# Optimization experiments

Hardware: AMD Instinct MI355X
Metric: run time of the kernel (lower is better)

The kernel has to match this reference:

```python
import jax, jax.numpy as jnp
import numpy as np

EPS = 1e-5      # BatchNorm eps (torch default)
TEMP = 2.0      # initial_temperature
TOP_K = 2


def _bn(x, g, b, m, v):
    # eval-mode BatchNorm over channel dim of [B, C]
    return (x - m) * jax.lax.rsqrt(v + EPS) * g + b


def setup_inputs() -> dict:
    key = jax.random.key(0)
    ks = jax.random.split(key, 16)
    B, C, H, W, E = 64, 768, 32, 32, 16
    C2 = 2 * C            # 1536
    R = C2 // 16          # 96 (ChannelAttention bottleneck)
    s = 0.02
    f32 = jnp.float32
    return {
        "x": jax.random.normal(ks[0], (B, C, H, W), f32),
        # conv1x1 C->2C
        "w1": jax.random.normal(ks[1], (C2, C), f32) * s,
        "b1": jnp.zeros((C2,), f32),
        # BN(2C)
        "bn1_g": jnp.ones((C2,), f32),
        "bn1_b": jnp.zeros((C2,), f32),
        "bn1_m": jax.random.normal(ks[2], (C2,), f32) * 0.1,
        "bn1_v": jax.random.uniform(ks[3], (C2,), f32, 0.5, 1.5),
        # ChannelAttention fc: 2C -> 2C/16 -> 2C
        "caw1": jax.random.normal(ks[4], (R, C2), f32) * s,
        "cab1": jnp.zeros((R,), f32),
        "caw2": jax.random.normal(ks[5], (C2, R), f32) * s,
        "cab2": jnp.zeros((C2,), f32),
        # conv1x1 2C->C
        "w2": jax.random.normal(ks[6], (C, C2), f32) * s,
        "b2": jnp.zeros((C,), f32),
        # BN(C)
        "bn2_g": jnp.ones((C,), f32),
        "bn2_b": jnp.zeros((C,), f32),
        "bn2_m": jax.random.normal(ks[7], (C,), f32) * 0.1,
        "bn2_v": jax.random.uniform(ks[8], (C,), f32, 0.5, 1.5),
        # conv1x1 C->E
        "w3": jax.random.normal(ks[9], (E, C), f32) * s,
        "b3": jnp.zeros((E,), f32),
    }


def reference(x, w1, b1, bn1_g, bn1_b, bn1_m, bn1_v,
              caw1, cab1, caw2, cab2,
              w2, b2, bn2_g, bn2_b, bn2_m, bn2_v,
              w3, b3):
    # global avg pool: [B,C,H,W] -> [B,C] (1x1 spatial squeezed)
    g = jnp.mean(x, axis=(2, 3))
    # conv1x1 C->2C + BN + GELU (exact erf gelu, torch default)
    h = jax.nn.gelu(_bn(g @ w1.T + b1, bn1_g, bn1_b, bn1_m, bn1_v),
                    approximate=False)
    # ChannelAttention on 1x1 feature map: avg_pool == max_pool == identity,
    # so avg_out + max_out = 2 * fc(h)
    a = jax.nn.gelu(h @ caw1.T + cab1, approximate=False) @ caw2.T + cab2
    h = h * jax.nn.sigmoid(a + a)
    # conv1x1 2C->C + BN + GELU
    h = jax.nn.gelu(_bn(h @ w2.T + b2, bn2_g, bn2_b, bn2_m, bn2_v),
                    approximate=False)
    # conv1x1 C->E -> gating scores [B, E]
    scores = h @ w3.T + b3
    vals, idx = jax.lax.top_k(scores, TOP_K)
    probs = jax.nn.softmax(vals / TEMP, axis=1)
    return idx, probs
```

## Files before the change

kernel.cpp:

```cpp
#include <hip/hip_runtime.h>
#include <hip/hip_bf16.h>
#include <math.h>

#define B_   64
#define C_   768
#define C2_  1536
#define R_   96
#define E_   16
#define HW_  1024

typedef float f32x4 __attribute__((ext_vector_type(4)));

__device__ __forceinline__ float gelu_exact(float x) {
    return 0.5f * x * (1.0f + erff(x * 0.70710678118654752440f));
}

__device__ __forceinline__ f32x4 nt_load4(const float* p) {
    return __builtin_nontemporal_load(reinterpret_cast<const f32x4*>(p));
}

__global__ __launch_bounds__(256) void pool_kernel(const float* __restrict__ x,
                                                   float* __restrict__ gT) {
    const int wave = threadIdx.x >> 6;
    const int lane = threadIdx.x & 63;
    const int row  = blockIdx.x * 4 + wave;
    const int b = row / C_;
    const int c = row % C_;
    const float* p = x + (size_t)row * HW_;
    f32x4 a0 = nt_load4(p + lane * 4 +    0);
    f32x4 a1 = nt_load4(p + lane * 4 +  256);
    f32x4 a2 = nt_load4(p + lane * 4 +  512);
    f32x4 a3 = nt_load4(p + lane * 4 +  768);
    float s = (a0.x + a0.y + a0.z + a0.w) + (a1.x + a1.y + a1.z + a1.w)
            + (a2.x + a2.y + a2.z + a2.w) + (a3.x + a3.y + a3.z + a3.w);
    #pragma unroll
    for (int off = 32; off >= 1; off >>= 1) s += __shfl_xor(s, off);
    if (lane == 0) gT[c * B_ + b] = s * (1.0f / (float)HW_);
}

template<int K, bool BN>
__global__ __launch_bounds__(512) void gemv4_kernel(
    const float* __restrict__ inT,
    const float* __restrict__ W,
    const float* __restrict__ bias,
    const float* __restrict__ bn_g, const float* __restrict__ bn_b,
    const float* __restrict__ bn_m, const float* __restrict__ bn_v,
    float* __restrict__ outT)
{
    __shared__ __align__(16) float wl[4 * K];
    __shared__ float part[4][8][64];
    const int t  = threadIdx.x;
    const int c0 = blockIdx.x * 4;
    {
        const float* src = W + (size_t)c0 * K;
        f32x4* dst = reinterpret_cast<f32x4*>(wl);
        #pragma unroll
        for (int i = t; i < K; i += 512) dst[i] = nt_load4(src + i * 4);
    }
    __syncthreads();
    const int b = t & 63, w = t >> 6;
    const int kc = w * (K / 8);
    const float* w0 = wl + kc;
    const float* g  = inT + (size_t)kc * B_ + b;
    float a0 = 0.f, a1 = 0.f, a2 = 0.f, a3 = 0.f;
    #pragma unroll 8
    for (int k = 0; k < K / 8; ++k) {
        float gv = g[k * B_];
        a0 = fmaf(gv, w0[k],         a0);
        a1 = fmaf(gv, w0[K + k],     a1);
        a2 = fmaf(gv, w0[2 * K + k], a2);
        a3 = fmaf(gv, w0[3 * K + k], a3);
    }
    part[0][w][b] = a0;
    part[1][w][b] = a1;
    part[2][w][b] = a2;
    part[3][w][b] = a3;
    __syncthreads();
    if (t < 256) {
        const int ci = t >> 6, bb = t & 63, c = c0 + ci;
        float s = (part[ci][0][bb] + part[ci][1][bb])
                + (part[ci][2][bb] + part[ci][3][bb])
                + (part[ci][4][bb] + part[ci][5][bb])
                + (part[ci][6][bb] + part[ci][7][bb]);
        s += bias[c];
        if (BN) s = (s - bn_m[c]) * rsqrtf(bn_v[c] + 1e-5f) * bn_g[c] + bn_b[c];
        outT[(size_t)c * B_ + bb] = gelu_exact(s);
    }
}

__global__ __launch_bounds__(512) void l2_kernel(
    const float* __restrict__ h1T, const float* __restrict__ caw1,
    const float* __restrict__ cab1, float* __restrict__ rT)
{
    __shared__ __align__(16) float wl[C2_];
    __shared__ float part[8][64];
    const int t = threadIdx.x;
    const int c = blockIdx.x;
    {
        const float* src = caw1 + (size_t)c * C2_;
        f32x4* dst = reinterpret_cast<f32x4*>(wl);
        if (t < 384) dst[t] = nt_load4(src + t * 4);
    }
    __syncthreads();
    const int b = t & 63, w = t >> 6;
    const int kc = w * 192;
    const float* hp = h1T + (size_t)kc * B_ + b;
    float a0 = 0.f, a1 = 0.f, a2 = 0.f;
    #pragma unroll 8
    for (int k = 0; k < 64; ++k) {
        a0 = fmaf(hp[k * B_],         wl[kc + k],       a0);
        a1 = fmaf(hp[(k + 64) * B_],  wl[kc + k + 64],  a1);
        a2 = fmaf(hp[(k + 128) * B_], wl[kc + k + 128], a2);
    }
    part[w][b] = (a0 + a1) + a2;
    __syncthreads();
    if (t < 64) {
        float s = 0.f;
        #pragma unroll
        for (int ww = 0; ww < 8; ++ww) s += part[ww][t];
        rT[(size_t)c * B_ + t] = gelu_exact(s + cab1[c]);
    }
}

__global__ __launch_bounds__(512) void gate_kernel(
    const float* __restrict__ rT, const float* __restrict__ caw2,
    const float* __restrict__ cab2,
    const float* __restrict__ h1T, float* __restrict__ h1gT)
{
    const int t = threadIdx.x;
    const int b = t & 63, w = t >> 6;
    const int c = __builtin_amdgcn_readfirstlane(blockIdx.x * 8 + w);
    const float* wr = caw2 + (size_t)c * R_;
    const float* rp = rT + b;
    float a0 = 0.f, a1 = 0.f;
    #pragma unroll 8
    for (int k = 0; k < 48; ++k) {
        a0 = fmaf(rp[k * B_],        wr[k],      a0);
        a1 = fmaf(rp[(k + 48) * B_], wr[k + 48], a1);
    }
    float a = a0 + a1 + cab2[c];
    float sig = 1.0f / (1.0f + expf(-2.0f * a));
    h1gT[(size_t)c * B_ + b] = h1T[(size_t)c * B_ + b] * sig;
}

__global__ __launch_bounds__(256) void l5_kernel(
    const float* __restrict__ h2T, const float* __restrict__ w3,
    const float* __restrict__ b3, float* __restrict__ out)
{
    __shared__ float part[256];
    __shared__ float sc[E_];
    const int t = threadIdx.x;
    const int b = blockIdx.x;
    const int e = t & 15, kg = t >> 4;
    const float* wr = w3 + (size_t)e * C_ + kg * 48;
    const float* hv = h2T + (size_t)kg * 48 * B_ + b;
    float acc = 0.f;
    #pragma unroll 8
    for (int j = 0; j < 48; ++j) acc = fmaf(hv[j * B_], wr[j], acc);
    part[t] = acc;
    __syncthreads();
    if (t < E_) {
        float s = b3[t];
        #pragma unroll
        for (int kgi = 0; kgi < 16; ++kgi) s += part[kgi * 16 + t];
        sc[t] = s;
    }
    __syncthreads();
    if (t == 0) {
        int i0 = 0; float v0 = sc[0];
        #pragma unroll
        for (int i = 1; i < E_; ++i) { if (sc[i] > v0) { v0 = sc[i]; i0 = i; } }
        int i1 = -1; float v1 = -INFINITY;
        #pragma unroll
        for (int i = 0; i < E_; ++i) {
            if (i == i0) continue;
            if (sc[i] > v1) { v1 = sc[i]; i1 = i; }
        }
        float e1 = expf((v1 - v0) * 0.5f);
        float inv = 1.0f / (1.0f + e1);
        out[b * 2 + 0] = (float)i0;
        out[b * 2 + 1] = (float)i1;
        out[2 * B_ + b * 2 + 0] = inv;
        out[2 * B_ + b * 2 + 1] = e1 * inv;
    }
}

extern "C" void kernel_launch(void* const* d_in, const int* in_sizes, int n_in,
                              void* d_out, int out_size, void* d_ws, size_t ws_size,
                              hipStream_t stream) {
    const float* x     = (const float*)d_in[0];
    const float* w1    = (const float*)d_in[1];
    const float* b1    = (const float*)d_in[2];
    const float* bn1_g = (const float*)d_in[3];
    const float* bn1_b = (const float*)d_in[4];
    const float* bn1_m = (const float*)d_in[5];
    const float* bn1_v = (const float*)d_in[6];
    const float* caw1  = (const float*)d_in[7];
    const float* cab1  = (const float*)d_in[8];
    const float* caw2  = (const float*)d_in[9];
    const float* cab2  = (const float*)d_in[10];
    const float* w2    = (const float*)d_in[11];
    const float* b2    = (const float*)d_in[12];
    const float* bn2_g = (const float*)d_in[13];
    const float* bn2_b = (const float*)d_in[14];
    const float* bn2_m = (const float*)d_in[15];
    const float* bn2_v = (const float*)d_in[16];
    const float* w3    = (const float*)d_in[17];
    const float* b3    = (const float*)d_in[18];

    float* ws   = (float*)d_ws;
    float* gT   = ws;
    float* h1T  = ws + 49152;
    float* rT   = ws + 147456;
    float* h2T  = ws + 153600;
    float* h1gT = ws + 202752;
    float* out = (float*)d_out;

    pool_kernel<<<(B_ * C_) / 4, 256, 0, stream>>>(x, gT);
    gemv4_kernel<C_, true><<<C2_ / 4, 512, 0, stream>>>(
        gT, w1, b1, bn1_g, bn1_b, bn1_m, bn1_v, h1T);
    l2_kernel<<<R_, 512, 0, stream>>>(h1T, caw1, cab1, rT);
    gate_kernel<<<C2_ / 8, 512, 0, stream>>>(rT, caw2, cab2, h1T, h1gT);
    gemv4_kernel<C2_, true><<<C_ / 4, 512, 0, stream>>>(
        h1gT, w2, b2, bn2_g, bn2_b, bn2_m, bn2_v, h2T);
    l5_kernel<<<B_, 256, 0, stream>>>(h2T, w3, b3, out);
}
```

Measured before the change: 66.33 us.

## Fuse channel-attention layers into one per-batch kernel with pre-transposed caw2

Replaces the separate l2 and gate kernels with a single ca_gate_kernel that runs one block per batch row. The block stages h1 in shared memory, computes the 96-wide bottleneck with wave reductions, then applies the gate. The caw2 transpose it needs is folded into extra blocks of the pool kernel so it costs no extra launch. This removes one launch and the rT round trip. The trade-off is only 64 blocks, with each block rereading caw1 and caw2T, which lowers parallelism and raises L2 traffic. The old path is kept as a fallback when the workspace is too small.

```diff
diff --git a/kernel.cpp b/kernel.cpp
--- a/kernel.cpp
+++ b/kernel.cpp
@@ -8,6 +8,8 @@
 #define R_   96
 #define E_   16
 #define HW_  1024
+#define POOLB_ (B_ * C_ / 4)
+#define TRB_   24
 
 typedef float f32x4 __attribute__((ext_vector_type(4)));
 
@@ -20,7 +22,19 @@
 }
 
 __global__ __launch_bounds__(256) void pool_kernel(const float* __restrict__ x,
-                                                   float* __restrict__ gT) {
+                                                   float* __restrict__ gT,
+                                                   const float* __restrict__ caw2,
+                                                   float* __restrict__ caw2T) {
+    if (blockIdx.x >= POOLB_) {
+        const int base = (blockIdx.x - POOLB_) * 6144 + threadIdx.x;
+        #pragma unroll 4
+        for (int n = 0; n < 24; ++n) {
+            int idx = base + n * 256;
+            int k = idx / C2_, c = idx - k * C2_;
+            caw2T[idx] = caw2[(size_t)c * R_ + k];
+        }
+        return;
+    }
     const int wave = threadIdx.x >> 6;
     const int lane = threadIdx.x & 63;
     const int row  = blockIdx.x * 4 + wave;
@@ -40,8 +54,7 @@
 
 template<int K, bool BN>
 __global__ __launch_bounds__(512) void gemv4_kernel(
-    const float* __restrict__ inT,
-    const float* __restrict__ W,
+    const float* __restrict__ inT, const float* __restrict__ W,
     const float* __restrict__ bias,
     const float* __restrict__ bn_g, const float* __restrict__ bn_b,
     const float* __restrict__ bn_m, const float* __restrict__ bn_v,
@@ -88,6 +101,45 @@
     }
 }
 
+__global__ __launch_bounds__(512) void ca_gate_kernel(
+    const float* __restrict__ h1T,
+    const float* __restrict__ caw1, const float* __restrict__ cab1,
+    const float* __restrict__ caw2T, const float* __restrict__ cab2,
+    float* __restrict__ h1gT)
+{
+    __shared__ float h1l[C2_];
+    __shared__ float rl[R_];
+    const int t = threadIdx.x;
+    const int b = blockIdx.x;
+    #pragma unroll
+    for (int i = 0; i < 3; ++i) h1l[t + i * 512] = h1T[(size_t)(t + i * 512) * B_ + b];
+    __syncthreads();
+    const int w = t >> 6, l = t & 63;
+    #pragma unroll
+    for (int jj = 0; jj < 12; ++jj) {
+        const int j = w * 12 + jj;
+        const float* wr = caw1 + (size_t)j * C2_;
+        float acc = 0.f;
+        #pragma unroll 8
+        for (int m = 0; m < 24; ++m)
+            acc = fmaf(wr[l + 64 * m], h1l[l + 64 * m], acc);
+        #pragma unroll
+        for (int off = 32; off >= 1; off >>= 1) acc += __shfl_xor(acc, off);
+        if (l == 0) rl[j] = gelu_exact(acc + cab1[j]);
+    }
+    __syncthreads();
+    #pragma unroll
+    for (int cc = 0; cc < 3; ++cc) {
+        const int c = t + cc * 512;
+        float a = cab2[c];
+        #pragma unroll 8
+        for (int k = 0; k < R_; ++k)
+            a = fmaf(caw2T[(size_t)k * C2_ + c], rl[k], a);
+        float sig = 1.0f / (1.0f + expf(-2.0f * a));
+        h1gT[(size_t)c * B_ + b] = h1l[c] * sig;
+    }
+}
+
 __global__ __launch_bounds__(512) void l2_kernel(
     const float* __restrict__ h1T, const float* __restrict__ caw1,
     const float* __restrict__ cab1, float* __restrict__ rT)
@@ -96,11 +148,7 @@
     __shared__ float part[8][64];
     const int t = threadIdx.x;
     const int c = blockIdx.x;
-    {
-        const float* src = caw1 + (size_t)c * C2_;
-        f32x4* dst = reinterpret_cast<f32x4*>(wl);
-        if (t < 384) dst[t] = nt_load4(src + t * 4);
-    }
+    if (t < 384) reinterpret_cast<f32x4*>(wl)[t] = nt_load4(caw1 + (size_t)c * C2_ + t * 4);
     __syncthreads();
     const int b = t & 63, w = t >> 6;
     const int kc = w * 192;
@@ -208,20 +256,33 @@
     const float* w3    = (const float*)d_in[17];
     const float* b3    = (const float*)d_in[18];
 
-    float* ws   = (float*)d_ws;
-    float* gT   = ws;
-    float* h1T  = ws + 49152;
-    float* rT   = ws + 147456;
-    float* h2T  = ws + 153600;
-    float* h1gT = ws + 202752;
+    float* ws    = (float*)d_ws;
+    float* gT    = ws;
+    float* h1T   = ws + 49152;
+    float* h1gT  = ws + 147456;
+    float* h2T   = ws + 245760;
+    float* caw2T = ws + 294912;
     float* out = (float*)d_out;
 
-    pool_kernel<<<(B_ * C_) / 4, 256, 0, stream>>>(x, gT);
-    gemv4_kernel<C_, true><<<C2_ / 4, 512, 0, stream>>>(
-        gT, w1, b1, bn1_g, bn1_b, bn1_m, bn1_v, h1T);
-    l2_kernel<<<R_, 512, 0, stream>>>(h1T, caw1, cab1, rT);
-    gate_kernel<<<C2_ / 8, 512, 0, stream>>>(rT, caw2, cab2, h1T, h1gT);
-    gemv4_kernel<C2_, true><<<C_ / 4, 512, 0, stream>>>(
-        h1gT, w2, b2, bn2_g, bn2_b, bn2_m, bn2_v, h2T);
-    l5_kernel<<<B_, 256, 0, stream>>>(h2T, w3, b3, out);
-}
+    if (ws_size >= (size_t)442368 * sizeof(float)) {
+        pool_kernel<<<POOLB_ + TRB_, 256, 0, stream>>>(x, gT, caw2, caw2T);
+        gemv4_kernel<C_, true><<<C2_ / 4, 512, 0, stream>>>(
+            gT, w1, b1, bn1_g, bn1_b, bn1_m, bn1_v, h1T);
+        ca_gate_kernel<<<B_, 512, 0, stream>>>(h1T, caw1, cab1, caw2T, cab2, h1gT);
+        gemv4_kernel<C2_, true><<<C_ / 4, 512, 0, stream>>>(
+            h1gT, w2, b2, bn2_g, bn2_b, bn2_m, bn2_v, h2T);
+        l5_kernel<<<B_, 256, 0, stream>>>(h2T, w3, b3, out);
+    } else {
+        float* rT    = ws + 147456;
+        float* h2Tf  = ws + 153600;
+        float* h1gTf = ws + 202752;
+        pool_kernel<<<POOLB_, 256, 0, stream>>>(x, gT, caw2, nullptr);
+        gemv4_kernel<C_, true><<<C2_ / 4, 512, 0, stream>>>(
+            gT, w1, b1, bn1_g, bn1_b, bn1_m, bn1_v, h1T);
+        l2_kernel<<<R_, 512, 0, stream>>>(h1T, caw1, cab1, rT);
+        gate_kernel<<<C2_ / 8, 512, 0, stream>>>(rT, caw2, cab2, h1T, h1gTf);
+        gemv4_kernel<C2_, true><<<C_ / 4, 512, 0, stream>>>(
+            h1gTf, w2, b2, bn2_g, bn2_b, bn2_m, bn2_v, h2Tf);
+        l5_kernel<<<B_, 256, 0, stream>>>(h2Tf, w3, b3, out);
+    }
+}
```

Result: slower. 90.21 us (+36.0%).
